# Kernel tuning notes

Measured on AMD Instinct MI355X. Metric: run time of the kernel, lower is better.

## Reference

```python
import jax, jax.numpy as jnp
import numpy as np

N, C, E, H = 50000, 128, 1_600_000, 32
JITTER = 1e-20


def _lin(k, fan_in, fan_out):
    return jax.random.normal(k, (fan_in, fan_out), jnp.float32) / np.sqrt(fan_in)


def setup_inputs() -> dict:
    key = jax.random.key(0)
    ks = jax.random.split(key, 20)
    x = jax.random.normal(ks[0], (N, C), jnp.float32)
    edge_index = jax.random.randint(ks[1], (2, E), 0, N, dtype=jnp.int64)
    inp = {"x": x, "edge_index": edge_index}
    # actor params
    inp["aW"] = _lin(ks[2], C, C); inp["ab"] = jnp.zeros((C,), jnp.float32)
    inp["a1W"] = _lin(ks[3], C, H); inp["a1b"] = jnp.zeros((H,), jnp.float32)
    inp["a2W"] = _lin(ks[4], H, H); inp["a2b"] = jnp.zeros((H,), jnp.float32)
    inp["a3W"] = _lin(ks[5], H, 2); inp["a3b"] = jnp.zeros((2,), jnp.float32)
    # critic params
    inp["cW"] = _lin(ks[6], C, C); inp["cb"] = jnp.zeros((C,), jnp.float32)
    inp["c1W"] = _lin(ks[7], C, H); inp["c1b"] = jnp.zeros((H,), jnp.float32)
    inp["c2W"] = _lin(ks[8], H, H); inp["c2b"] = jnp.zeros((H,), jnp.float32)
    inp["c3W"] = _lin(ks[9], H, 2); inp["c3b"] = jnp.zeros((2,), jnp.float32)
    return inp


def gcn_conv(x, src, dst, W, b):
    """Standard PyG GCNConv: add self-loops, symmetric degree norm, X@W, scatter-add, +bias."""
    n = x.shape[0]
    loop = jnp.arange(n)
    s = jnp.concatenate([src, loop])  # [E+N]
    d = jnp.concatenate([dst, loop])
    deg = jax.ops.segment_sum(jnp.ones_like(d, jnp.float32), d, num_segments=n)
    dinv = jnp.where(deg > 0, jax.lax.rsqrt(deg), 0.0)
    norm = dinv[s] * dinv[d]                     # [E+N]
    h = x @ W                                    # [N, C]
    agg = jax.ops.segment_sum(h[s] * norm[:, None], d, num_segments=n)
    return agg + b


def reference(x, edge_index, aW, ab, a1W, a1b, a2W, a2b, a3W, a3b,
              cW, cb, c1W, c1b, c2W, c2b, c3W, c3b):
    src, dst = edge_index[0], edge_index[1]
    # actor
    h = jax.nn.relu(gcn_conv(x, src, dst, aW, ab)) + x
    h = jax.nn.relu(h @ a1W + a1b)
    h = jax.nn.relu(h @ a2W + a2b)
    a = h @ a3W + a3b                            # [N, 2]
    concentration = jax.nn.softplus(a[:, 0]) + JITTER
    p = jax.nn.softplus(a[:, 1])
    action2_probs = p / jnp.sum(p)
    # critic
    hc = jax.nn.relu(gcn_conv(x, src, dst, cW, cb)) + x
    hc = jnp.sum(hc, axis=0)                     # [C]
    hc = jax.nn.relu(hc @ c1W + c1b)
    hc = jax.nn.relu(hc @ c2W + c2b)
    value = hc @ c3W + c3b                       # [2]
    return (concentration, value, action2_probs)
```

## Files before the change

### kernel.cpp

```cpp
#include <hip/hip_runtime.h>
#include <hip/hip_bf16.h>
#include <hip/hip_fp16.h>
#include <math.h>

#define C 128
#define BCAP 12288

using half8x = __attribute__((ext_vector_type(8))) _Float16;
using half4x = __attribute__((ext_vector_type(4))) _Float16;
using f32x4  = __attribute__((ext_vector_type(4))) float;

__device__ inline float4 h4_to_f4(uint2 u) {
    __half2 p0 = *(__half2*)&u.x;
    __half2 p1 = *(__half2*)&u.y;
    float2 f0 = __half22float2(p0), f1 = __half22float2(p1);
    return make_float4(f0.x, f0.y, f1.x, f1.y);
}

__device__ inline float softplusf(float v) {
    return (v > 20.f) ? v : log1pf(expf(v));
}

__global__ __launch_bounds__(256) void wtk(const float* __restrict__ aW, const float* __restrict__ cW,
                                           const float* __restrict__ a1W,
                                           __half* __restrict__ wt, __half* __restrict__ a1wt,
                                           unsigned* gcur, float* colsum, float* pSum) {
    int t = threadIdx.x;
    if (blockIdx.x == 0) {
        gcur[t] = 0u;
        if (t < 128) colsum[t] = 0.f;
        if (t == 128) pSum[0] = 0.f;
    }
    int idx = blockIdx.x * 256 + t;
    if (idx < 32768) {
        int y = idx >> 14, r = idx & 16383;
        int k = r >> 7, n = r & 127;
        const float* W = y ? cW : aW;
        wt[((size_t)y << 14) + n * 128 + k] = __float2half(W[k * 128 + n]);
    } else if (idx < 36864) {
        int r = idx - 32768;
        int k = r >> 5, n = r & 31;
        a1wt[n * 128 + k] = __float2half(a1W[k * 32 + n]);
    }
}

__global__ __launch_bounds__(256) void bink(const int* __restrict__ ei,
                                            unsigned* __restrict__ gcur,
                                            unsigned* __restrict__ gstage,
                                            int E, int NBKT) {
    __shared__ unsigned raw[6400];
    __shared__ unsigned image[6400];
    __shared__ unsigned cnt[256];
    __shared__ unsigned pref[256];
    __shared__ unsigned cur[256];
    __shared__ unsigned gb[256];
    int t = threadIdx.x, b = blockIdx.x;
    int elo = (int)((long long)b * E / 256);
    int ehi = (int)((long long)(b + 1) * E / 256);
    int n = ehi - elo;

    for (int i = t; i < n; i += 256) {
        int d = __builtin_nontemporal_load(ei + E + elo + i);
        int s = __builtin_nontemporal_load(ei + elo + i);
        raw[i] = (unsigned)s | ((unsigned)(d & 255) << 16) | ((unsigned)(d >> 8) << 24);
    }
    cnt[t] = 0u; cur[t] = 0u;
    __syncthreads();
    for (int i = t; i < n; i += 256) atomicAdd(&cnt[raw[i] >> 24], 1u);
    __syncthreads();
    pref[t] = cnt[t];
    __syncthreads();
    for (int off = 1; off < 256; off <<= 1) {
        unsigned add = (t >= off) ? pref[t - off] : 0u;
        __syncthreads();
        pref[t] += add;
        __syncthreads();
    }
    gb[t] = (t < NBKT && cnt[t]) ? atomicAdd(&gcur[t], cnt[t]) : 0u;
    __syncthreads();
    for (int i = t; i < n; i += 256) {
        unsigned v = raw[i];
        unsigned B = v >> 24;
        unsigned pos = (pref[B] - cnt[B]) + atomicAdd(&cur[B], 1u);
        image[pos] = v & 0xFFFFFFu;
    }
    __syncthreads();
    int wv = t >> 6, lane = t & 63;
    for (int B = wv; B < NBKT; B += 4) {
        unsigned c = cnt[B];
        if (!c) continue;
        unsigned eb = pref[B] - c;
        unsigned gbase = gb[B];
        unsigned c2 = (gbase < BCAP) ? ((c < BCAP - gbase) ? c : BCAP - gbase) : 0u;
        for (unsigned i = lane; i < c2; i += 64)
            gstage[(size_t)B * BCAP + gbase + i] = image[eb + i];
    }
}

__global__ __launch_bounds__(256) void placek(const unsigned* __restrict__ gstage,
                                              const unsigned* __restrict__ gcur,
                                              int* __restrict__ rowptr, float* __restrict__ dinv,
                                              int* __restrict__ col, int N, int NBKT) {
    __shared__ unsigned image[BCAP];
    __shared__ unsigned cnt[256];
    __shared__ unsigned pref[256];
    __shared__ unsigned cur[256];
    __shared__ unsigned sbase[256];
    int B = blockIdx.x, t = threadIdx.x;

    unsigned gv = (t < NBKT) ? gcur[t] : 0u;
    unsigned val = (gv < BCAP) ? gv : BCAP;
    sbase[t] = val;
    __syncthreads();
    for (int off = 1; off < 256; off <<= 1) {
        unsigned add = (t >= off) ? sbase[t - off] : 0u;
        __syncthreads();
        sbase[t] += add;
        __syncthreads();
    }
    unsigned gB = gcur[B];
    unsigned m = (gB < BCAP) ? gB : BCAP;
    unsigned base = sbase[B] - m;
    const unsigned* st = gstage + (size_t)B * BCAP;

    cnt[t] = 0u; cur[t] = 0u;
    __syncthreads();
    for (unsigned i = t; i < m; i += 256) atomicAdd(&cnt[(st[i] >> 16) & 255u], 1u);
    __syncthreads();
    pref[t] = cnt[t];
    __syncthreads();
    for (int off = 1; off < 256; off <<= 1) {
        unsigned add = (t >= off) ? pref[t - off] : 0u;
        __syncthreads();
        pref[t] += add;
        __syncthreads();
    }
    int d = B * 256 + t;
    if (d < N) {
        rowptr[d] = (int)(base + pref[t] - cnt[t]);
        dinv[d] = rsqrtf((float)(cnt[t] + 1u));
    }
    if (B == NBKT - 1 && t == 0) rowptr[N] = (int)(base + m);
    for (unsigned i = t; i < m; i += 256) {
        unsigned v = st[i];
        unsigned dl = (v >> 16) & 255u;
        unsigned pos = (pref[dl] - cnt[dl]) + atomicAdd(&cur[dl], 1u);
        image[pos] = v & 0xFFFFu;
    }
    __syncthreads();
    for (unsigned i = t; i < m; i += 256) col[base + i] = (int)image[i];
}

__global__ __launch_bounds__(256) void xhk(const float* __restrict__ x, const float* __restrict__ dinv,
                                           __half* __restrict__ xh, __half* __restrict__ x16, int N) {
    int i = blockIdx.x * 256 + threadIdx.x;
    if (i >= N * 64) return;
    int node = i >> 6, fp = (i & 63) * 2;
    float w = dinv[node];
    float2 f = *(const float2*)&x[(size_t)node * C + fp];
    __half2 h = __floats2half2_rn(f.x * w, f.y * w);
    __half2 hx = __floats2half2_rn(f.x, f.y);
    *(unsigned*)&xh[(size_t)node * C + fp] = *(unsigned*)&h;
    *(unsigned*)&x16[(size_t)node * C + fp] = *(unsigned*)&hx;
}

__global__ __launch_bounds__(256) void gatherk(const int* __restrict__ col,
                                               const int* __restrict__ rowptr,
                                               const __half* __restrict__ xh,
                                               const float* __restrict__ dinv,
                                               __half* __restrict__ gg, int N) {
    __shared__ int snb[4][64];
    int t = threadIdx.x;
    int wid = t >> 6, lane = t & 63;
    int d = blockIdx.x * 4 + wid;
    if (d >= N) return;
    int beg = rowptr[d], end = rowptr[d + 1];
    int half = lane >> 5, sub = lane & 31;
    int f = sub * 4;

    float a0 = 0.f, a1 = 0.f, a2 = 0.f, a3 = 0.f;

    for (int c = beg; c < end; c += 64) {
        if (c + lane < end) snb[wid][lane] = __builtin_nontemporal_load(col + c + lane);
        int n = end - c; if (n > 64) n = 64;
        int j = 0;
        for (; j + 3 < n; j += 4) {
            size_t i0 = (size_t)snb[wid][j + half] * C + f;
            size_t i1 = (size_t)snb[wid][j + 2 + half] * C + f;
            float4 v0 = h4_to_f4(*(const uint2*)&xh[i0]);
            float4 v1 = h4_to_f4(*(const uint2*)&xh[i1]);
            a0 += v0.x + v1.x;
            a1 += v0.y + v1.y;
            a2 += v0.z + v1.z;
            a3 += v0.w + v1.w;
        }
        for (; j < n; j += 2) {
            if (j + half < n) {
                float4 v = h4_to_f4(*(const uint2*)&xh[(size_t)snb[wid][j + half] * C + f]);
                a0 += v.x; a1 += v.y; a2 += v.z; a3 += v.w;
            }
        }
    }
    a0 += __shfl_xor(a0, 32, 64);
    a1 += __shfl_xor(a1, 32, 64);
    a2 += __shfl_xor(a2, 32, 64);
    a3 += __shfl_xor(a3, 32, 64);

    if (half == 0) {
        float4 s4 = h4_to_f4(*(const uint2*)&xh[(size_t)d * C + f]);
        float dv = dinv[d];
        __half2 h0 = __floats2half2_rn((a0 + s4.x) * dv, (a1 + s4.y) * dv);
        __half2 h1 = __floats2half2_rn((a2 + s4.z) * dv, (a3 + s4.w) * dv);
        uint2 u; u.x = *(unsigned*)&h0; u.y = *(unsigned*)&h1;
        *(uint2*)&gg[(size_t)d * C + f] = u;
    }
}

__global__ __launch_bounds__(256) void gemm2k(const __half* __restrict__ gg,
                                              const __half* __restrict__ wt,
                                              const __half* __restrict__ a1wt,
                                              const float* __restrict__ ab, const float* __restrict__ cb,
                                              const __half* __restrict__ x16,
                                              const float* __restrict__ a1b,
                                              const float* __restrict__ a2W, const float* __restrict__ a2b,
                                              const float* __restrict__ a3W, const float* __restrict__ a3b,
                                              float* __restrict__ scratch,
                                              float* __restrict__ out, float* __restrict__ pSum, int N) {
    __shared__ char As[8192];
    __shared__ char Act[8192];
    __shared__ char Aux[5888];
    _Float16* w2t = (_Float16*)Aux;
    _Float16* h1b = (_Float16*)(Aux + 2560);
    float* w3s    = (float*)(Aux + 5120);
    float* scol   = (float*)(Aux + 5376);

    const int row0 = blockIdx.x * 32;
    const int t = threadIdx.x;
    const int wv = t >> 6, l = t & 63;
    const int lm = l & 15, lk = l >> 4;
    const int koffB = lk * 16;
    const int koffH = lk * 8;

    uint2 xpre[2][2];
#pragma unroll
    for (int rg = 0; rg < 2; ++rg) {
        int grow = row0 + rg * 16 + lm;
#pragma unroll
        for (int nc2 = 0; nc2 < 2; ++nc2) {
            int nc = wv * 2 + nc2;
            xpre[rg][nc2] = (grow < N) ? *(const uint2*)&x16[(size_t)grow * C + nc * 16 + lk * 4]
                                       : make_uint2(0u, 0u);
        }
    }

#pragma unroll
    for (int i = 0; i < 2; ++i) {
        int c = t + i * 256;
        int row = c >> 4, cb16 = (c & 15) * 16;
        int grow = row0 + row;
        uint4 u = make_uint4(0u, 0u, 0u, 0u);
        if (grow < N) u = *(const uint4*)&gg[(size_t)grow * C + (c & 15) * 8];
        *(uint4*)(As + row * 256 + (cb16 ^ ((row & 7) << 4))) = u;
    }
#pragma unroll
    for (int i = 0; i < 4; ++i) {
        int idx = t + i * 256;
        int k = idx >> 5, n = idx & 31;
        w2t[n * 40 + k] = (_Float16)a2W[idx];
    }
    if (t < 64) w3s[t] = a3W[t];
    __syncthreads();

    const __half* WA = wt;
    const __half* WC = wt + 16384;

#pragma unroll
    for (int nc2 = 0; nc2 < 2; ++nc2) {
        const int nc = wv * 2 + nc2;
        const __half* wpA = WA + (nc * 16 + lm) * 128;
        const __half* wpC = WC + (nc * 16 + lm) * 128;
        half8x bfA[4], bfC[4];
#pragma unroll
        for (int kc = 0; kc < 4; ++kc) {
            bfA[kc] = *(const half8x*)(wpA + kc * 32 + koffH);
            bfC[kc] = *(const half8x*)(wpC + kc * 32 + koffH);
        }
        float4 bvA = *(const float4*)&ab[nc * 16 + lk * 4];
        float4 bvC = *(const float4*)&cb[nc * 16 + lk * 4];
        float v0 = 0.f, v1 = 0.f, v2 = 0.f, v3 = 0.f;

#pragma unroll
        for (int rg = 0; rg < 2; ++rg) {
            int rowA = rg * 16 + lm;
            int grow = row0 + rowA;
            bool valid = grow < N;
            int sw = (rowA & 7) << 4;
            const char* rp = As + rowA * 256;
            f32x4 accA = {0.f, 0.f, 0.f, 0.f};
            f32x4 accC = {0.f, 0.f, 0.f, 0.f};
#pragma unroll
            for (int kc = 0; kc < 4; ++kc) {
                half8x afr = *(const half8x*)(rp + ((kc * 64 + koffB) ^ sw));
                accA = __builtin_amdgcn_mfma_f32_16x16x32_f16(bfA[kc], afr, accA, 0, 0, 0);
                accC = __builtin_amdgcn_mfma_f32_16x16x32_f16(bfC[kc], afr, accC, 0, 0, 0);
            }
            half4x xq = *(half4x*)&xpre[rg][nc2];
            half4x hv = { (_Float16)(valid ? fmaxf(accA[0] + bvA.x, 0.f) + (float)xq[0] : 0.f),
                          (_Float16)(valid ? fmaxf(accA[1] + bvA.y, 0.f) + (float)xq[1] : 0.f),
                          (_Float16)(valid ? fmaxf(accA[2] + bvA.z, 0.f) + (float)xq[2] : 0.f),
                          (_Float16)(valid ? fmaxf(accA[3] + bvA.w, 0.f) + (float)xq[3] : 0.f) };
            *(half4x*)(Act + rowA * 256 + ((nc * 32 + lk * 8) ^ sw)) = hv;
            v0 += valid ? fmaxf(accC[0] + bvC.x, 0.f) + (float)xq[0] : 0.f;
            v1 += valid ? fmaxf(accC[1] + bvC.y, 0.f) + (float)xq[1] : 0.f;
            v2 += valid ? fmaxf(accC[2] + bvC.z, 0.f) + (float)xq[2] : 0.f;
            v3 += valid ? fmaxf(accC[3] + bvC.w, 0.f) + (float)xq[3] : 0.f;
        }
        v0 += __shfl_xor(v0, 1, 64); v0 += __shfl_xor(v0, 2, 64);
        v0 += __shfl_xor(v0, 4, 64); v0 += __shfl_xor(v0, 8, 64);
        v1 += __shfl_xor(v1, 1, 64); v1 += __shfl_xor(v1, 2, 64);
        v1 += __shfl_xor(v1, 4, 64); v1 += __shfl_xor(v1, 8, 64);
        v2 += __shfl_xor(v2, 1, 64); v2 += __shfl_xor(v2, 2, 64);
        v2 += __shfl_xor(v2, 4, 64); v2 += __shfl_xor(v2, 8, 64);
        v3 += __shfl_xor(v3, 1, 64); v3 += __shfl_xor(v3, 2, 64);
        v3 += __shfl_xor(v3, 4, 64); v3 += __shfl_xor(v3, 8, 64);
        if (lm == 0)
            *(float4*)&scol[nc * 16 + lk * 4] = make_float4(v0, v1, v2, v3);
    }
    __syncthreads();

    if (t < 128)
        scratch[(size_t)blockIdx.x * 128 + t] = scol[t];

    if (wv < 2) {
        const int rowM = wv * 16 + lm;
        const int growM = row0 + rowM;
        const bool validM = growM < N;
        const int swM = (rowM & 7) << 4;

        half8x a1f[4];
        {
            const char* rp = Act + rowM * 256;
#pragma unroll
            for (int kc = 0; kc < 4; ++kc)
                a1f[kc] = *(const half8x*)(rp + ((kc * 64 + koffB) ^ swM));
        }
#pragma unroll
        for (int ct = 0; ct < 2; ++ct) {
            const __half* ap = a1wt + (ct * 16 + lm) * 128;
            f32x4 acc1 = {0.f, 0.f, 0.f, 0.f};
#pragma unroll
            for (int kc = 0; kc < 4; ++kc) {
                half8x bq = *(const half8x*)(ap + kc * 32 + koffH);
                acc1 = __builtin_amdgcn_mfma_f32_16x16x32_f16(bq, a1f[kc], acc1, 0, 0, 0);
            }
            float4 b1v = *(const float4*)&a1b[ct * 16 + lk * 4];
            half4x h = { (_Float16)fmaxf(acc1[0] + b1v.x, 0.f),
                         (_Float16)fmaxf(acc1[1] + b1v.y, 0.f),
                         (_Float16)fmaxf(acc1[2] + b1v.z, 0.f),
                         (_Float16)fmaxf(acc1[3] + b1v.w, 0.f) };
            *(half4x*)((char*)h1b + rowM * 80 + ct * 32 + lk * 8) = h;
        }

        half4x alo = *(const half4x*)((char*)h1b + rowM * 80 + lk * 16);
        half4x ahi = *(const half4x*)((char*)h1b + rowM * 80 + lk * 16 + 8);
        half8x a2f = __builtin_shufflevector(alo, ahi, 0, 1, 2, 3, 4, 5, 6, 7);
        float p0 = 0.f, p1 = 0.f;
#pragma unroll
        for (int ct = 0; ct < 2; ++ct) {
            half4x blo = *(const half4x*)((char*)w2t + (ct * 16 + lm) * 80 + lk * 16);
            half4x bhi = *(const half4x*)((char*)w2t + (ct * 16 + lm) * 80 + lk * 16 + 8);
            half8x b2f = __builtin_shufflevector(blo, bhi, 0, 1, 2, 3, 4, 5, 6, 7);
            f32x4 acc2 = {0.f, 0.f, 0.f, 0.f};
            acc2 = __builtin_amdgcn_mfma_f32_16x16x32_f16(b2f, a2f, acc2, 0, 0, 0);
            float4 b2v = *(const float4*)&a2b[ct * 16 + lk * 4];
#pragma unroll
            for (int j = 0; j < 4; ++j) {
                int f = ct * 16 + lk * 4 + j;
                float h2v = fmaxf(acc2[j] + (&b2v.x)[j], 0.f);
                float2 w3 = *(const float2*)&w3s[f * 2];
                p0 += h2v * w3.x;
                p1 += h2v * w3.y;
            }
        }
        p0 += __shfl_xor(p0, 16, 64); p0 += __shfl_xor(p0, 32, 64);
        p1 += __shfl_xor(p1, 16, 64); p1 += __shfl_xor(p1, 32, 64);
        float wave_psum = 0.f;
        if (lk == 0 && validM) {
            float s0 = softplusf(p0 + a3b[0]);
            float s1 = softplusf(p1 + a3b[1]);
            out[growM] = s0 + 1e-20f;
            out[(size_t)N + 2 + growM] = s1;
            wave_psum = s1;
        }
        wave_psum += __shfl_xor(wave_psum, 1, 64);
        wave_psum += __shfl_xor(wave_psum, 2, 64);
        wave_psum += __shfl_xor(wave_psum, 4, 64);
        wave_psum += __shfl_xor(wave_psum, 8, 64);
        wave_psum += __shfl_xor(wave_psum, 16, 64);
        wave_psum += __shfl_xor(wave_psum, 32, 64);
        if (l == 0) atomicAdd(pSum, wave_psum);
    }
}

__global__ __launch_bounds__(128) void csredk(const float* __restrict__ scratch, float* __restrict__ colsum, int nblk) {
    int t = threadIdx.x;
    float s = 0.f;
    for (int b = blockIdx.x; b < nblk; b += gridDim.x)
        s += scratch[(size_t)b * 128 + t];
    atomicAdd(&colsum[t], s);
}

__global__ void critick(const float* __restrict__ colsum,
                        const float* __restrict__ c1W, const float* __restrict__ c1b,
                        const float* __restrict__ c2W, const float* __restrict__ c2b,
                        const float* __restrict__ c3W, const float* __restrict__ c3b,
                        float* __restrict__ out, int N) {
    __shared__ float s1[32], s2[32];
    int t = threadIdx.x;
    if (t < 32) {
        float acc = c1b[t];
        for (int k = 0; k < 128; ++k) acc += colsum[k] * c1W[k * 32 + t];
        s1[t] = fmaxf(acc, 0.f);
    }
    __syncthreads();
    if (t < 32) {
        float acc = c2b[t];
        for (int k = 0; k < 32; ++k) acc += s1[k] * c2W[k * 32 + t];
        s2[t] = fmaxf(acc, 0.f);
    }
    __syncthreads();
    if (t < 2) {
        float acc = c3b[t];
        for (int k = 0; k < 32; ++k) acc += s2[k] * c3W[k * 2 + t];
        out[(size_t)N + t] = acc;
    }
}

__global__ __launch_bounds__(256) void normk(float* __restrict__ out, const float* __restrict__ pSum, int N) {
    int i = blockIdx.x * 256 + threadIdx.x;
    if (i < N) out[(size_t)N + 2 + i] /= pSum[0];
}

extern "C" void kernel_launch(void* const* d_in, const int* in_sizes, int n_in,
                              void* d_out, int out_size, void* d_ws, size_t ws_size,
                              hipStream_t stream) {
    const float* x   = (const float*)d_in[0];
    const int* ei    = (const int*)d_in[1];
    const float* aW  = (const float*)d_in[2];
    const float* ab  = (const float*)d_in[3];
    const float* a1W = (const float*)d_in[4];
    const float* a1b = (const float*)d_in[5];
    const float* a2W = (const float*)d_in[6];
    const float* a2b = (const float*)d_in[7];
    const float* a3W = (const float*)d_in[8];
    const float* a3b = (const float*)d_in[9];
    const float* cW  = (const float*)d_in[10];
    const float* cb  = (const float*)d_in[11];
    const float* c1W = (const float*)d_in[12];
    const float* c1b = (const float*)d_in[13];
    const float* c2W = (const float*)d_in[14];
    const float* c2b = (const float*)d_in[15];
    const float* c3W = (const float*)d_in[16];
    const float* c3b = (const float*)d_in[17];

    const int N = in_sizes[0] / C;
    const int E = in_sizes[1] / 2;
    const int NBKT = (N + 255) / 256;
    const int nblk32 = (N + 31) / 32;
    float* out = (float*)d_out;

    char* ws = (char*)d_ws;
    size_t off = 0;
    auto alloc = [&](size_t bytes) {
        size_t o = off;
        off = (off + bytes + 255) & ~(size_t)255;
        return (void*)(ws + o);
    };
    unsigned* gcur    = (unsigned*)alloc(256 * 4);
    unsigned* gstage  = (unsigned*)alloc((size_t)NBKT * BCAP * 4);
    int* rowptr       = (int*)alloc((size_t)(N + 1) * 4);
    float* dinv       = (float*)alloc((size_t)N * 4);
    int* colidx       = (int*)alloc((size_t)E * 4);
    __half* xh        = (__half*)alloc((size_t)N * C * 2);
    __half* x16       = (__half*)alloc((size_t)N * C * 2);
    __half* gg        = (__half*)alloc((size_t)N * C * 2);
    __half* wt        = (__half*)alloc(2 * 16384 * 2);
    __half* a1wt      = (__half*)alloc(4096 * 2);
    float* scratch    = (float*)alloc((size_t)nblk32 * 128 * 4);
    float* colsum     = (float*)alloc(128 * 4);
    float* pSum       = (float*)alloc(4);

    wtk<<<144, 256, 0, stream>>>(aW, cW, a1W, wt, a1wt, gcur, colsum, pSum);
    bink<<<256, 256, 0, stream>>>(ei, gcur, gstage, E, NBKT);
    placek<<<NBKT, 256, 0, stream>>>(gstage, gcur, rowptr, dinv, colidx, N, NBKT);
    xhk<<<(N * 64 + 255) / 256, 256, 0, stream>>>(x, dinv, xh, x16, N);
    gatherk<<<(N + 3) / 4, 256, 0, stream>>>(colidx, rowptr, xh, dinv, gg, N);
    gemm2k<<<nblk32, 256, 0, stream>>>(gg, wt, a1wt, ab, cb, x16,
                                       a1b, a2W, a2b, a3W, a3b,
                                       scratch, out, pSum, N);
    csredk<<<8, 128, 0, stream>>>(scratch, colsum, nblk32);
    critick<<<1, 64, 0, stream>>>(colsum, c1W, c1b, c2W, c2b, c3W, c3b, out, N);
    normk<<<(N + 255) / 256, 256, 0, stream>>>(out, pSum, N);
}
```

Baseline: 230.4 us.

## Fuse neighbor gather into GEMM kernel, writing aggregated rows directly to LDS

The separate gather kernel is removed. Each GEMM block of 32 rows now performs the sparse neighbor aggregation itself, with each wave handling 8 destination rows serially, and writes the fp16 results straight into the swizzled shared-memory A tile. This drops the gg intermediate buffer (a global write and a re-read of N×C halves) and one kernel launch. In exchange, gather parallelism falls from about 12.5k blocks to about 1.5k blocks, so latency hiding for the random xh reads may be weaker.

```diff
diff --git a/kernel.cpp b/kernel.cpp
--- a/kernel.cpp
+++ b/kernel.cpp
@@ -164,71 +164,23 @@
     *(unsigned*)&x16[(size_t)node * C + fp] = *(unsigned*)&hx;
 }
 
-__global__ __launch_bounds__(256) void gatherk(const int* __restrict__ col,
-                                               const int* __restrict__ rowptr,
-                                               const __half* __restrict__ xh,
-                                               const float* __restrict__ dinv,
-                                               __half* __restrict__ gg, int N) {
-    __shared__ int snb[4][64];
-    int t = threadIdx.x;
-    int wid = t >> 6, lane = t & 63;
-    int d = blockIdx.x * 4 + wid;
-    if (d >= N) return;
-    int beg = rowptr[d], end = rowptr[d + 1];
-    int half = lane >> 5, sub = lane & 31;
-    int f = sub * 4;
-
-    float a0 = 0.f, a1 = 0.f, a2 = 0.f, a3 = 0.f;
-
-    for (int c = beg; c < end; c += 64) {
-        if (c + lane < end) snb[wid][lane] = __builtin_nontemporal_load(col + c + lane);
-        int n = end - c; if (n > 64) n = 64;
-        int j = 0;
-        for (; j + 3 < n; j += 4) {
-            size_t i0 = (size_t)snb[wid][j + half] * C + f;
-            size_t i1 = (size_t)snb[wid][j + 2 + half] * C + f;
-            float4 v0 = h4_to_f4(*(const uint2*)&xh[i0]);
-            float4 v1 = h4_to_f4(*(const uint2*)&xh[i1]);
-            a0 += v0.x + v1.x;
-            a1 += v0.y + v1.y;
-            a2 += v0.z + v1.z;
-            a3 += v0.w + v1.w;
-        }
-        for (; j < n; j += 2) {
-            if (j + half < n) {
-                float4 v = h4_to_f4(*(const uint2*)&xh[(size_t)snb[wid][j + half] * C + f]);
-                a0 += v.x; a1 += v.y; a2 += v.z; a3 += v.w;
-            }
-        }
-    }
-    a0 += __shfl_xor(a0, 32, 64);
-    a1 += __shfl_xor(a1, 32, 64);
-    a2 += __shfl_xor(a2, 32, 64);
-    a3 += __shfl_xor(a3, 32, 64);
-
-    if (half == 0) {
-        float4 s4 = h4_to_f4(*(const uint2*)&xh[(size_t)d * C + f]);
-        float dv = dinv[d];
-        __half2 h0 = __floats2half2_rn((a0 + s4.x) * dv, (a1 + s4.y) * dv);
-        __half2 h1 = __floats2half2_rn((a2 + s4.z) * dv, (a3 + s4.w) * dv);
-        uint2 u; u.x = *(unsigned*)&h0; u.y = *(unsigned*)&h1;
-        *(uint2*)&gg[(size_t)d * C + f] = u;
-    }
-}
-
-__global__ __launch_bounds__(256) void gemm2k(const __half* __restrict__ gg,
-                                              const __half* __restrict__ wt,
-                                              const __half* __restrict__ a1wt,
-                                              const float* __restrict__ ab, const float* __restrict__ cb,
-                                              const __half* __restrict__ x16,
-                                              const float* __restrict__ a1b,
-                                              const float* __restrict__ a2W, const float* __restrict__ a2b,
-                                              const float* __restrict__ a3W, const float* __restrict__ a3b,
-                                              float* __restrict__ scratch,
-                                              float* __restrict__ out, float* __restrict__ pSum, int N) {
+__global__ __launch_bounds__(256) void ggemk(const int* __restrict__ col,
+                                             const int* __restrict__ rowptr,
+                                             const __half* __restrict__ xh,
+                                             const float* __restrict__ dinv,
+                                             const __half* __restrict__ wt,
+                                             const __half* __restrict__ a1wt,
+                                             const float* __restrict__ ab, const float* __restrict__ cb,
+                                             const __half* __restrict__ x16,
+                                             const float* __restrict__ a1b,
+                                             const float* __restrict__ a2W, const float* __restrict__ a2b,
+                                             const float* __restrict__ a3W, const float* __restrict__ a3b,
+                                             float* __restrict__ scratch,
+                                             float* __restrict__ out, float* __restrict__ pSum, int N) {
     __shared__ char As[8192];
     __shared__ char Act[8192];
     __shared__ char Aux[5888];
+    __shared__ int  snb[4][64];
     _Float16* w2t = (_Float16*)Aux;
     _Float16* h1b = (_Float16*)(Aux + 2560);
     float* w3s    = (float*)(Aux + 5120);
@@ -254,21 +206,64 @@
     }
 
 #pragma unroll
-    for (int i = 0; i < 2; ++i) {
-        int c = t + i * 256;
-        int row = c >> 4, cb16 = (c & 15) * 16;
-        int grow = row0 + row;
-        uint4 u = make_uint4(0u, 0u, 0u, 0u);
-        if (grow < N) u = *(const uint4*)&gg[(size_t)grow * C + (c & 15) * 8];
-        *(uint4*)(As + row * 256 + (cb16 ^ ((row & 7) << 4))) = u;
-    }
-#pragma unroll
     for (int i = 0; i < 4; ++i) {
         int idx = t + i * 256;
         int k = idx >> 5, n = idx & 31;
         w2t[n * 40 + k] = (_Float16)a2W[idx];
     }
     if (t < 64) w3s[t] = a3W[t];
+
+    {
+        int half = l >> 5, sub = l & 31;
+        int fB = sub * 8;
+        int fH = sub * 4;
+        for (int i = 0; i < 8; ++i) {
+            int rowA = wv * 8 + i;
+            int d = row0 + rowA;
+            int sw = (rowA & 7) << 4;
+            float a0 = 0.f, a1 = 0.f, a2 = 0.f, a3 = 0.f;
+            if (d < N) {
+                int beg = rowptr[d], end = rowptr[d + 1];
+                for (int c = beg; c < end; c += 64) {
+                    if (c + l < end) snb[wv][l] = __builtin_nontemporal_load(col + c + l);
+                    int n = end - c; if (n > 64) n = 64;
+                    int j = 0;
+                    for (; j + 3 < n; j += 4) {
+                        size_t i0 = (size_t)snb[wv][j + half] * C + fH;
+                        size_t i1 = (size_t)snb[wv][j + 2 + half] * C + fH;
+                        float4 v0 = h4_to_f4(*(const uint2*)&xh[i0]);
+                        float4 v1 = h4_to_f4(*(const uint2*)&xh[i1]);
+                        a0 += v0.x + v1.x;
+                        a1 += v0.y + v1.y;
+                        a2 += v0.z + v1.z;
+                        a3 += v0.w + v1.w;
+                    }
+                    for (; j < n; j += 2) {
+                        if (j + half < n) {
+                            float4 v = h4_to_f4(*(const uint2*)&xh[(size_t)snb[wv][j + half] * C + fH]);
+                            a0 += v.x; a1 += v.y; a2 += v.z; a3 += v.w;
+                        }
+                    }
+                }
+                a0 += __shfl_xor(a0, 32, 64);
+                a1 += __shfl_xor(a1, 32, 64);
+                a2 += __shfl_xor(a2, 32, 64);
+                a3 += __shfl_xor(a3, 32, 64);
+                if (half == 0) {
+                    float4 s4 = h4_to_f4(*(const uint2*)&xh[(size_t)d * C + fH]);
+                    float dv = dinv[d];
+                    half4x hv = { (_Float16)((a0 + s4.x) * dv),
+                                  (_Float16)((a1 + s4.y) * dv),
+                                  (_Float16)((a2 + s4.z) * dv),
+                                  (_Float16)((a3 + s4.w) * dv) };
+                    *(half4x*)(As + rowA * 256 + (fB ^ sw)) = hv;
+                }
+            } else if (half == 0) {
+                half4x z = {};
+                *(half4x*)(As + rowA * 256 + (fB ^ sw)) = z;
+            }
+        }
+    }
     __syncthreads();
 
     const __half* WA = wt;
@@ -483,7 +478,6 @@
     int* colidx       = (int*)alloc((size_t)E * 4);
     __half* xh        = (__half*)alloc((size_t)N * C * 2);
     __half* x16       = (__half*)alloc((size_t)N * C * 2);
-    __half* gg        = (__half*)alloc((size_t)N * C * 2);
     __half* wt        = (__half*)alloc(2 * 16384 * 2);
     __half* a1wt      = (__half*)alloc(4096 * 2);
     float* scratch    = (float*)alloc((size_t)nblk32 * 128 * 4);
@@ -494,10 +488,9 @@
     bink<<<256, 256, 0, stream>>>(ei, gcur, gstage, E, NBKT);
     placek<<<NBKT, 256, 0, stream>>>(gstage, gcur, rowptr, dinv, colidx, N, NBKT);
     xhk<<<(N * 64 + 255) / 256, 256, 0, stream>>>(x, dinv, xh, x16, N);
-    gatherk<<<(N + 3) / 4, 256, 0, stream>>>(colidx, rowptr, xh, dinv, gg, N);
-    gemm2k<<<nblk32, 256, 0, stream>>>(gg, wt, a1wt, ab, cb, x16,
-                                       a1b, a2W, a2b, a3W, a3b,
-                                       scratch, out, pSum, N);
+    ggemk<<<nblk32, 256, 0, stream>>>(colidx, rowptr, xh, dinv, wt, a1wt, ab, cb, x16,
+                                      a1b, a2W, a2b, a3W, a3b,
+                                      scratch, out, pSum, N);
     csredk<<<8, 128, 0, stream>>>(scratch, colsum, nblk32);
     critick<<<1, 64, 0, stream>>>(colsum, c1W, c1b, c2W, c2b, c3W, c3b, out, N);
     normk<<<(N + 255) / 256, 256, 0, stream>>>(out, pSum, N);
```

After: 248.3 us. +7.8%, slower.
